# Kernel optimization log

Hardware: AMD Instinct MI355X
Metric: run time of the kernel (lower is better)

The kernel has to match this reference:

```python
import jax, jax.numpy as jnp
import numpy as np
import math


def _instance_cl(z1, z2):
    # z1, z2: [B, T, C] -> per-element instance contrastive loss [B, T]
    B = z1.shape[0]
    z = jnp.concatenate([z1, z2], axis=0)          # [2B, T, C]
    z = z.transpose(1, 0, 2)                        # [T, 2B, C]
    sim = jnp.einsum('tic,tjc->tij', z, z)          # [T, 2B, 2B]
    # drop diagonal: tril(-1) shifted + triu(1) shifted -> [T, 2B, 2B-1]
    logits = jnp.tril(sim, -1)[:, :, :-1] + jnp.triu(sim, 1)[:, :, 1:]
    logits = -jax.nn.log_softmax(logits, axis=-1)
    i = jnp.arange(B)
    loss = (logits[:, i, B + i - 1] + logits[:, B + i, i]) / 2.0   # [T, B]
    return loss.T                                    # [B, T]


def _temporal_cl(z1, z2):
    # z1, z2: [B, T, C] -> per-timestep temporal contrastive loss [B, T]
    T = z1.shape[1]
    z = jnp.concatenate([z1, z2], axis=1)            # [B, 2T, C]
    sim = jnp.einsum('bic,bjc->bij', z, z)           # [B, 2T, 2T]
    logits = jnp.tril(sim, -1)[:, :, :-1] + jnp.triu(sim, 1)[:, :, 1:]
    logits = -jax.nn.log_softmax(logits, axis=-1)
    t = jnp.arange(T)
    return (logits[:, t, T + t - 1] + logits[:, T + t, t]) / 2.0   # [B, T]


def _contrastive_corr(z1, z2, alpha=0.5):
    # per-(batch, timestep) contrastive score, shape [B, L]
    return alpha * _instance_cl(z1, z2) + (1.0 - alpha) * _temporal_cl(z1, z2)


def setup_inputs() -> dict:
    key = jax.random.key(0)
    k1, k2, k3 = jax.random.split(key, 3)
    B, L, H, E = 4, 2048, 8, 64
    queries = jax.random.normal(k1, (B, L, H, E), dtype=jnp.float32)
    keys = jax.random.normal(k2, (B, L, H, E), dtype=jnp.float32)
    values = jax.random.normal(k3, (B, L, H, E), dtype=jnp.float32)
    attn_mask = jnp.zeros((1,), dtype=bool)  # unused; ProbMask is rebuilt internally
    return {"queries": queries, "keys": keys, "values": values, "attn_mask": attn_mask}


FACTOR = 1.0


def reference(queries, keys, values, attn_mask):
    B, L, H, E = queries.shape
    # S == L here so key/value slicing branch is a no-op
    corr = _contrastive_corr(queries.reshape(B, L, H * E),
                             keys.reshape(B, L, H * E))       # [B, L]
    top_k = int(FACTOR * math.log(L))                          # static (=7 for L=2048)
    _, index = jax.lax.top_k(corr.mean(axis=0), top_k)         # [K]
    corr_top = corr[:, index]                                  # [B, K]
    # scores[b,h,k,l] = corr_top[b,k] broadcast over h and l
    scores = jnp.broadcast_to(corr_top[:, None, :, None], (B, H, top_k, L))
    # ProbMask: mask future positions l > index[k] (causal for the selected queries)
    mask = jnp.arange(L)[None, :] > index[:, None]             # [K, L]
    scores = jnp.where(mask[None, None, :, :], -jnp.inf, scores)
    attn = jax.nn.softmax(scores, axis=-1)                     # [B, H, K, L]
    V = values.transpose(0, 2, 1, 3)                           # [B, H, L, D]
    context = jnp.cumsum(V, axis=2)                            # initial context (mask_flag=True)
    out = jnp.einsum('bhkl,bhld->bhkd', attn, V)               # [B, H, K, D]
    context = context.at[:, :, index, :].set(out)              # scatter update
    return context
```

## Files before the change

kernel.cpp:

```cpp
#include <hip/hip_runtime.h>
#include <math.h>


typedef __attribute__((ext_vector_type(8))) short short8;
typedef __attribute__((ext_vector_type(8))) unsigned short ushort8;
typedef __attribute__((ext_vector_type(4))) float f32x4;

typedef const __attribute__((address_space(1))) void* gas_ptr;
typedef __attribute__((address_space(3))) void* las_ptr;

#define EXP_OFF 80.0f

__device__ __forceinline__ void async_cp16(const void* g, void* l) {
  __builtin_amdgcn_global_load_lds((gas_ptr)g, (las_ptr)l, 16, 0, 0);
}

__device__ __forceinline__ unsigned short f2bf(float x) {
  union { float f; unsigned int u; } v; v.f = x;
  unsigned int r = v.u + 0x7FFFu + ((v.u >> 16) & 1u);
  return (unsigned short)(r >> 16);
}

__global__ __launch_bounds__(256) void convert_bf16_kernel(
    const float* __restrict__ Q, const float* __restrict__ K,
    unsigned short* __restrict__ Z) {
  int tid = blockIdx.x * 256 + threadIdx.x;
  int row = tid >> 6;
  int c0 = (tid & 63) * 8;
  int b = row >> 12, i = row & 4095;
  const float* src = (i < 2048)
      ? Q + ((size_t)(b * 2048 + i) * 512 + c0)
      : K + ((size_t)(b * 2048 + (i - 2048)) * 512 + c0);
  float4 v0 = ((const float4*)src)[0];
  float4 v1 = ((const float4*)src)[1];
  ushort8 o;
  o[0] = f2bf(v0.x); o[1] = f2bf(v0.y); o[2] = f2bf(v0.z); o[3] = f2bf(v0.w);
  o[4] = f2bf(v1.x); o[5] = f2bf(v1.y); o[6] = f2bf(v1.z); o[7] = f2bf(v1.w);
  *(ushort8*)(Z + (size_t)row * 512 + c0) = o;
}

__global__ __launch_bounds__(256, 3) void temporal_gemm_kernel(
    const unsigned short* __restrict__ Z, float* __restrict__ part) {
  int id = blockIdx.x;
  int b = id / 528;
  int t = id - b * 528;
  int cj = (int)((sqrtf(8.0f * (float)t + 1.0f) - 1.0f) * 0.5f);
  while ((cj + 1) * (cj + 2) / 2 <= t) cj++;
  while (cj * (cj + 1) / 2 > t) cj--;
  int ri = t - cj * (cj + 1) / 2;
  const unsigned short* Zb = Z + (size_t)b * 4096 * 512;

  __shared__ __align__(16) unsigned short As[128 * 32];
  __shared__ __align__(16) unsigned short Bs[128 * 32];

  int tid = threadIdx.x;
  int w = tid >> 6, lane = tid & 63;
  int wr = w >> 1, wc = w & 1;
  int lm = lane & 15, q = lane >> 4;
  int swz = q ^ ((lm >> 1) & 3);

  int srow = lane >> 2;
  int kq = (lane & 3) ^ ((lane >> 3) & 3);
  int rl0 = w * 16 + srow;
  int rl1 = 64 + rl0;
  const unsigned short* gA0 = Zb + (size_t)(ri * 128 + rl0) * 512 + kq * 8;
  const unsigned short* gA1 = Zb + (size_t)(ri * 128 + rl1) * 512 + kq * 8;
  const unsigned short* gB0 = Zb + (size_t)(cj * 128 + rl0) * 512 + kq * 8;
  const unsigned short* gB1 = Zb + (size_t)(cj * 128 + rl1) * 512 + kq * 8;
  unsigned short* lA0 = As + (w * 16) * 32;
  unsigned short* lA1 = As + (64 + w * 16) * 32;
  unsigned short* lB0 = Bs + (w * 16) * 32;
  unsigned short* lB1 = Bs + (64 + w * 16) * 32;

  f32x4 acc[4][4];
#pragma unroll
  for (int mi = 0; mi < 4; mi++)
#pragma unroll
    for (int ni = 0; ni < 4; ni++) acc[mi][ni] = (f32x4)(0.f);

  for (int kc = 0; kc < 16; ++kc) {
    int go = kc * 32;
    async_cp16(gA0 + go, lA0);
    async_cp16(gA1 + go, lA1);
    async_cp16(gB0 + go, lB0);
    async_cp16(gB1 + go, lB1);
    __syncthreads();

    short8 af[4], bfr[4];
#pragma unroll
    for (int mi = 0; mi < 4; mi++) {
      int ar = wr * 64 + mi * 16 + lm;
      af[mi] = *(const short8*)(As + ar * 32 + swz * 8);
    }
#pragma unroll
    for (int ni = 0; ni < 4; ni++) {
      int bc = wc * 64 + ni * 16 + lm;
      bfr[ni] = *(const short8*)(Bs + bc * 32 + swz * 8);
    }
#pragma unroll
    for (int mi = 0; mi < 4; mi++)
#pragma unroll
      for (int ni = 0; ni < 4; ni++)
        acc[mi][ni] = __builtin_amdgcn_mfma_f32_16x16x32_bf16(
            af[mi], bfr[ni], acc[mi][ni], 0, 0, 0);
    __syncthreads();
  }

  float rsum[4][4];
  float csum[4];
#pragma unroll
  for (int mi = 0; mi < 4; mi++)
#pragma unroll
    for (int rr = 0; rr < 4; rr++) rsum[mi][rr] = 0.f;
#pragma unroll
  for (int ni = 0; ni < 4; ni++) csum[ni] = 0.f;

#pragma unroll
  for (int mi = 0; mi < 4; mi++) {
#pragma unroll
    for (int ni = 0; ni < 4; ni++) {
#pragma unroll
      for (int rr = 0; rr < 4; rr++) {
        int R = ri * 128 + wr * 64 + mi * 16 + q * 4 + rr;
        int Cg = cj * 128 + wc * 64 + ni * 16 + lm;
        float e = (R != Cg) ? __expf(acc[mi][ni][rr] - EXP_OFF) : 0.f;
        rsum[mi][rr] += e;
        csum[ni] += e;
      }
    }
  }

#pragma unroll
  for (int mi = 0; mi < 4; mi++) {
#pragma unroll
    for (int rr = 0; rr < 4; rr++) {
      float s = rsum[mi][rr];
      s += __shfl_xor(s, 1);
      s += __shfl_xor(s, 2);
      s += __shfl_xor(s, 4);
      s += __shfl_xor(s, 8);
      if (lm == 0) {
        int R = ri * 128 + wr * 64 + mi * 16 + q * 4 + rr;
        part[((size_t)(b * 4096 + R)) * 64 + cj * 2 + wc] = s;
      }
    }
  }

  if (ri != cj) {
#pragma unroll
    for (int ni = 0; ni < 4; ni++) {
      float s = csum[ni];
      s += __shfl_xor(s, 16);
      s += __shfl_xor(s, 32);
      if (q == 0) {
        int Cg = cj * 128 + wc * 64 + ni * 16 + lm;
        part[((size_t)(b * 4096 + Cg)) * 64 + ri * 2 + wr] = s;
      }
    }
  }
}

__global__ __launch_bounds__(256) void merge_row_kernel(
    const float* __restrict__ part, float* __restrict__ lse_temp) {
  int row = blockIdx.x * 256 + threadIdx.x;
  const float4* p = (const float4*)(part + (size_t)row * 64);
  float s = 0.f;
#pragma unroll
  for (int i = 0; i < 16; i++) {
    float4 v = p[i];
    s += v.x + v.y + v.z + v.w;
  }
  lse_temp[row] = EXP_OFF + __logf(s);
}

__global__ __launch_bounds__(256) void instance_kernel(
    const unsigned short* __restrict__ Z,
    float* __restrict__ lse_inst ,
    float* __restrict__ posdot ) {
  int wave = (blockIdx.x * 256 + threadIdx.x) >> 6;
  int t0 = wave * 2;
  int lane = threadIdx.x & 63;
  int lm = lane & 15, q = lane >> 4;
  int tt = (lm < 8) ? t0 : t0 + 1;
  int v = lm & 7;
  size_t zrow = (v < 4) ? ((size_t)v * 4096 + tt)
                        : ((size_t)(v - 4) * 4096 + 2048 + tt);
  const unsigned short* g = Z + zrow * 512 + q * 8;

  f32x4 acc0 = (f32x4)(0.f), acc1 = (f32x4)(0.f);
#pragma unroll
  for (int kc = 0; kc < 16; kc += 2) {
    short8 a0 = *(const short8*)(g + kc * 32);
    short8 a1 = *(const short8*)(g + kc * 32 + 32);
    acc0 = __builtin_amdgcn_mfma_f32_16x16x32_bf16(a0, a0, acc0, 0, 0, 0);
    acc1 = __builtin_amdgcn_mfma_f32_16x16x32_bf16(a1, a1, acc1, 0, 0, 0);
  }
  f32x4 acc = acc0 + acc1;

#pragma unroll
  for (int rr = 0; rr < 4; rr++) {
    int i = q * 4 + rr;
    float val = acc[rr];
    bool samehalf = ((i < 8) == (lm < 8));
    int t = (i < 8) ? t0 : t0 + 1;
    int iv = i & 7;
    if (samehalf && iv < 4 && (lm & 7) == iv + 4)
      posdot[iv * 2048 + t] = val;
    float dd = (samehalf && lm != i) ? val : -INFINITY;
    float mt = dd;
    mt = fmaxf(mt, __shfl_xor(mt, 1));
    mt = fmaxf(mt, __shfl_xor(mt, 2));
    mt = fmaxf(mt, __shfl_xor(mt, 4));
    float e = __expf(dd - mt);
    e += __shfl_xor(e, 1);
    e += __shfl_xor(e, 2);
    e += __shfl_xor(e, 4);
    if ((lm & 7) == 0 && samehalf) lse_inst[t * 8 + iv] = mt + __logf(e);
  }
}

__global__ __launch_bounds__(256) void combine_topk_kernel(
    const float* __restrict__ lse_inst, const float* __restrict__ lse_temp,
    const float* __restrict__ posdot, int* __restrict__ index_out) {
  __shared__ float wmax[4];
  __shared__ int widx[4];
  int tid = threadIdx.x;
  int base = tid * 8;
  float v[8];
#pragma unroll
  for (int r = 0; r < 8; r++) {
    int t = base + r;
    float sum = 0.f;
#pragma unroll
    for (int b = 0; b < 4; b++) {
      sum += 0.25f * (lse_inst[t * 8 + b] + lse_inst[t * 8 + 4 + b] +
                      lse_temp[b * 4096 + t] + lse_temp[b * 4096 + 2048 + t]) -
             posdot[b * 2048 + t];
    }
    v[r] = sum * 0.25f;
  }
  int lane = tid & 63, w = tid >> 6;
  for (int k = 0; k < 7; k++) {
    float bv = v[0];
    int bi = base;
#pragma unroll
    for (int r = 1; r < 8; r++)
      if (v[r] > bv) { bv = v[r]; bi = base + r; }
#pragma unroll
    for (int d = 1; d < 64; d <<= 1) {
      float ov = __shfl_xor(bv, d);
      int oi = __shfl_xor(bi, d);
      if (ov > bv || (ov == bv && oi < bi)) { bv = ov; bi = oi; }
    }
    if (lane == 0) { wmax[w] = bv; widx[w] = bi; }
    __syncthreads();
    float BV = wmax[0];
    int BI = widx[0];
#pragma unroll
    for (int ww = 1; ww < 4; ww++)
      if (wmax[ww] > BV || (wmax[ww] == BV && widx[ww] < BI)) {
        BV = wmax[ww];
        BI = widx[ww];
      }
    if (tid == 0) index_out[k] = BI;
    if (BI >= base && BI < base + 8) v[BI - base] = -INFINITY;
    __syncthreads();
  }
}

__global__ __launch_bounds__(64) void cumsum_phase1(const float* __restrict__ V,
                                                    float* __restrict__ partial) {
  int blk = blockIdx.x;
  int chunk = blk & 63;
  int bh = blk >> 6;
  int h = bh & 7, b = bh >> 3;
  int e = threadIdx.x;
  float s = 0.f;
  int l0 = chunk * 32;
  for (int l = l0; l < l0 + 32; l++)
    s += V[((size_t)(b * 2048 + l) * 8 + h) * 64 + e];
  partial[blk * 64 + e] = s;
}

__global__ __launch_bounds__(64) void cumsum_phase2(const float* __restrict__ V,
                                                    const float* __restrict__ partial,
                                                    const int* __restrict__ index,
                                                    float* __restrict__ out) {
  int blk = blockIdx.x;
  int chunk = blk & 63;
  int bh = blk >> 6;
  int h = bh & 7, b = bh >> 3;
  int e = threadIdx.x;
  float run = 0.f;
  for (int c = 0; c < chunk; c++) run += partial[(bh * 64 + c) * 64 + e];
  int idx[7];
#pragma unroll
  for (int k = 0; k < 7; k++) idx[k] = index[k];
  int l0 = chunk * 32;
  for (int l = l0; l < l0 + 32; l++) {
    run += V[((size_t)(b * 2048 + l) * 8 + h) * 64 + e];
    float o = run;
    bool special = false;
#pragma unroll
    for (int k = 0; k < 7; k++) special = special || (idx[k] == l);
    if (special) o = run / (float)(l + 1);
    out[((size_t)bh * 2048 + l) * 64 + e] = o;
  }
}

extern "C" void kernel_launch(void* const* d_in, const int* in_sizes, int n_in,
                              void* d_out, int out_size, void* d_ws, size_t ws_size,
                              hipStream_t stream) {
  const float* Q = (const float*)d_in[0];
  const float* K = (const float*)d_in[1];
  const float* V = (const float*)d_in[2];
  float* out = (float*)d_out;

  unsigned short* Z = (unsigned short*)d_ws;
  float* base = (float*)d_ws + 4 * 4096 * 512 / 2;
  float* part = base;
  float* lse_t = base + 4 * 4096 * 64;
  float* lse_i = lse_t + 16384;
  float* posd = lse_i + 16384;
  int* idx = (int*)(posd + 8192);
  float* cpart = posd + 8192 + 8;

  convert_bf16_kernel<<<4096, 256, 0, stream>>>(Q, K, Z);
  temporal_gemm_kernel<<<4 * 528, 256, 0, stream>>>(Z, part);
  instance_kernel<<<256, 256, 0, stream>>>(Z, lse_i, posd);
  merge_row_kernel<<<64, 256, 0, stream>>>(part, lse_t);
  combine_topk_kernel<<<1, 256, 0, stream>>>(lse_i, lse_t, posd, idx);
  cumsum_phase1<<<2048, 64, 0, stream>>>(V, cpart);
  cumsum_phase2<<<2048, 64, 0, stream>>>(V, cpart, idx, out);
}
```

Before: 199.2 us.

## Double-buffer temporal GEMM LDS loads, remap blocks, fuse cumsum into one kernel

The temporal GEMM now double-buffers its LDS tiles, prefetching the next K-chunk while running MFMAs on the current one, which removes one barrier per iteration. Block indices are remapped so that batches are interleaved. The two-phase cumsum is fused into a single kernel with one 1024-thread block per (b,h), sharing chunk partials through LDS. This saves a launch and a workspace round trip, but only 32 blocks run, with long serial strided loops that may underuse memory bandwidth.

```diff
diff --git a/kernel.cpp b/kernel.cpp
--- a/kernel.cpp
+++ b/kernel.cpp
@@ -42,16 +42,17 @@
 __global__ __launch_bounds__(256, 3) void temporal_gemm_kernel(
     const unsigned short* __restrict__ Z, float* __restrict__ part) {
   int id = blockIdx.x;
-  int b = id / 528;
-  int t = id - b * 528;
+  int x = id & 7;
+  int b = x >> 1;
+  int t = (id >> 3) * 2 + (x & 1);
   int cj = (int)((sqrtf(8.0f * (float)t + 1.0f) - 1.0f) * 0.5f);
   while ((cj + 1) * (cj + 2) / 2 <= t) cj++;
   while (cj * (cj + 1) / 2 > t) cj--;
   int ri = t - cj * (cj + 1) / 2;
   const unsigned short* Zb = Z + (size_t)b * 4096 * 512;
 
-  __shared__ __align__(16) unsigned short As[128 * 32];
-  __shared__ __align__(16) unsigned short Bs[128 * 32];
+  __shared__ __align__(16) unsigned short As[2][128 * 32];
+  __shared__ __align__(16) unsigned short Bs[2][128 * 32];
 
   int tid = threadIdx.x;
   int w = tid >> 6, lane = tid & 63;
@@ -67,10 +68,8 @@
   const unsigned short* gA1 = Zb + (size_t)(ri * 128 + rl1) * 512 + kq * 8;
   const unsigned short* gB0 = Zb + (size_t)(cj * 128 + rl0) * 512 + kq * 8;
   const unsigned short* gB1 = Zb + (size_t)(cj * 128 + rl1) * 512 + kq * 8;
-  unsigned short* lA0 = As + (w * 16) * 32;
-  unsigned short* lA1 = As + (64 + w * 16) * 32;
-  unsigned short* lB0 = Bs + (w * 16) * 32;
-  unsigned short* lB1 = Bs + (64 + w * 16) * 32;
+  int lo0 = (w * 16) * 32;
+  int lo1 = (64 + w * 16) * 32;
 
   f32x4 acc[4][4];
 #pragma unroll
@@ -78,24 +77,33 @@
 #pragma unroll
     for (int ni = 0; ni < 4; ni++) acc[mi][ni] = (f32x4)(0.f);
 
+  async_cp16(gA0, As[0] + lo0);
+  async_cp16(gA1, As[0] + lo1);
+  async_cp16(gB0, Bs[0] + lo0);
+  async_cp16(gB1, Bs[0] + lo1);
+
   for (int kc = 0; kc < 16; ++kc) {
-    int go = kc * 32;
-    async_cp16(gA0 + go, lA0);
-    async_cp16(gA1 + go, lA1);
-    async_cp16(gB0 + go, lB0);
-    async_cp16(gB1 + go, lB1);
+    int cur = kc & 1;
     __syncthreads();
+
+    if (kc < 15) {
+      int go = (kc + 1) * 32;
+      async_cp16(gA0 + go, As[cur ^ 1] + lo0);
+      async_cp16(gA1 + go, As[cur ^ 1] + lo1);
+      async_cp16(gB0 + go, Bs[cur ^ 1] + lo0);
+      async_cp16(gB1 + go, Bs[cur ^ 1] + lo1);
+    }
 
     short8 af[4], bfr[4];
 #pragma unroll
     for (int mi = 0; mi < 4; mi++) {
       int ar = wr * 64 + mi * 16 + lm;
-      af[mi] = *(const short8*)(As + ar * 32 + swz * 8);
+      af[mi] = *(const short8*)(As[cur] + ar * 32 + swz * 8);
     }
 #pragma unroll
     for (int ni = 0; ni < 4; ni++) {
       int bc = wc * 64 + ni * 16 + lm;
-      bfr[ni] = *(const short8*)(Bs + bc * 32 + swz * 8);
+      bfr[ni] = *(const short8*)(Bs[cur] + bc * 32 + swz * 8);
     }
 #pragma unroll
     for (int mi = 0; mi < 4; mi++)
@@ -103,7 +111,6 @@
       for (int ni = 0; ni < 4; ni++)
         acc[mi][ni] = __builtin_amdgcn_mfma_f32_16x16x32_bf16(
             af[mi], bfr[ni], acc[mi][ni], 0, 0, 0);
-    __syncthreads();
   }
 
   float rsum[4][4];
@@ -268,43 +275,43 @@
   }
 }
 
-__global__ __launch_bounds__(64) void cumsum_phase1(const float* __restrict__ V,
-                                                    float* __restrict__ partial) {
-  int blk = blockIdx.x;
-  int chunk = blk & 63;
-  int bh = blk >> 6;
+__global__ __launch_bounds__(1024) void cumsum_kernel(
+    const float* __restrict__ V, const int* __restrict__ index,
+    float* __restrict__ out) {
+  int bh = blockIdx.x;
   int h = bh & 7, b = bh >> 3;
-  int e = threadIdx.x;
+  int tid = threadIdx.x;
+  int e = tid & 63, c = tid >> 6;
+  __shared__ float psum[16][64];
+
+  const float* Vbase = V + (size_t)(b * 2048) * 512 + h * 64 + e;
+  float* obase = out + (size_t)bh * 2048 * 64 + e;
+
+  int l0 = c * 128;
   float s = 0.f;
-  int l0 = chunk * 32;
-  for (int l = l0; l < l0 + 32; l++)
-    s += V[((size_t)(b * 2048 + l) * 8 + h) * 64 + e];
-  partial[blk * 64 + e] = s;
-}
-
-__global__ __launch_bounds__(64) void cumsum_phase2(const float* __restrict__ V,
-                                                    const float* __restrict__ partial,
-                                                    const int* __restrict__ index,
-                                                    float* __restrict__ out) {
-  int blk = blockIdx.x;
-  int chunk = blk & 63;
-  int bh = blk >> 6;
-  int h = bh & 7, b = bh >> 3;
-  int e = threadIdx.x;
+  for (int l = l0; l < l0 + 128; ++l) s += Vbase[(size_t)l * 512];
+  psum[c][e] = s;
+
+  int idx[7];
+#pragma unroll
+  for (int k = 0; k < 7; k++) idx[k] = index[k];
+  __syncthreads();
+
   float run = 0.f;
-  for (int c = 0; c < chunk; c++) run += partial[(bh * 64 + c) * 64 + e];
-  int idx[7];
-#pragma unroll
-  for (int k = 0; k < 7; k++) idx[k] = index[k];
-  int l0 = chunk * 32;
-  for (int l = l0; l < l0 + 32; l++) {
-    run += V[((size_t)(b * 2048 + l) * 8 + h) * 64 + e];
+#pragma unroll
+  for (int cc = 0; cc < 16; ++cc) {
+    float p = psum[cc][e];
+    if (cc < c) run += p;
+  }
+
+  for (int l = l0; l < l0 + 128; ++l) {
+    run += Vbase[(size_t)l * 512];
     float o = run;
     bool special = false;
 #pragma unroll
     for (int k = 0; k < 7; k++) special = special || (idx[k] == l);
     if (special) o = run / (float)(l + 1);
-    out[((size_t)bh * 2048 + l) * 64 + e] = o;
+    obase[(size_t)l * 64] = o;
   }
 }
 
@@ -323,13 +330,11 @@
   float* lse_i = lse_t + 16384;
   float* posd = lse_i + 16384;
   int* idx = (int*)(posd + 8192);
-  float* cpart = posd + 8192 + 8;
 
   convert_bf16_kernel<<<4096, 256, 0, stream>>>(Q, K, Z);
   temporal_gemm_kernel<<<4 * 528, 256, 0, stream>>>(Z, part);
   instance_kernel<<<256, 256, 0, stream>>>(Z, lse_i, posd);
   merge_row_kernel<<<64, 256, 0, stream>>>(part, lse_t);
   combine_topk_kernel<<<1, 256, 0, stream>>>(lse_i, lse_t, posd, idx);
-  cumsum_phase1<<<2048, 64, 0, stream>>>(V, cpart);
-  cumsum_phase2<<<2048, 64, 0, stream>>>(V, cpart, idx, out);
-}
+  cumsum_kernel<<<32, 1024, 0, stream>>>(V, idx, out);
+}
```

After: 193.1 us. -3.1%, faster.
